# Kernel tuning notes

Measured on AMD Instinct MI355X. Metric: run time of the kernel, lower is better.

Reference implementation:

```python
import jax, jax.numpy as jnp
import numpy as np

B, L, E, H, NUM_USERS = 4096, 64, 384, 256, 10000
EPS = 1e-5


def _ln(x, g, b):
    m = jnp.mean(x, axis=-1, keepdims=True)
    v = jnp.mean((x - m) ** 2, axis=-1, keepdims=True)
    return g * (x - m) / jnp.sqrt(v + EPS) + b


def setup_inputs() -> dict:
    key = jax.random.key(0)
    ks = iter(jax.random.split(key, 32))
    inp = {}
    inp['user_ids'] = jax.random.randint(next(ks), (B,), 0, NUM_USERS)
    inp['query_embeddings'] = jax.random.normal(next(ks), (B, E), dtype=jnp.float32)
    inp['llm_embeddings'] = jax.random.normal(next(ks), (L, E), dtype=jnp.float32)
    inp['emb_table'] = jax.random.normal(next(ks), (NUM_USERS, E), dtype=jnp.float32) * 0.02
    # GNN layer 0 projections (E->H) for user/query/llm node types
    s0 = 1.0 / np.sqrt(E)
    for t in ('u', 'q', 'l'):
        inp[f'W{t}0'] = jax.random.uniform(next(ks), (E, H), jnp.float32, -s0, s0)
        inp[f'b{t}0'] = jnp.zeros((H,), jnp.float32)
    inp['g0'] = jnp.ones((H,), jnp.float32)
    inp['be0'] = jnp.zeros((H,), jnp.float32)
    # GNN layer 1 projections (H->H)
    s1 = 1.0 / np.sqrt(H)
    for t in ('u', 'q', 'l'):
        inp[f'W{t}1'] = jax.random.uniform(next(ks), (H, H), jnp.float32, -s1, s1)
        inp[f'b{t}1'] = jnp.zeros((H,), jnp.float32)
    inp['g1'] = jnp.ones((H,), jnp.float32)
    inp['be1'] = jnp.zeros((H,), jnp.float32)
    # prediction MLP: Linear(2H->H), ReLU, Linear(H->1)
    s2 = 1.0 / np.sqrt(2 * H)
    inp['w1'] = jax.random.uniform(next(ks), (2 * H, H), jnp.float32, -s2, s2)
    inp['b1'] = jnp.zeros((H,), jnp.float32)
    s3 = 1.0 / np.sqrt(H)
    inp['w2'] = jax.random.uniform(next(ks), (H, 1), jnp.float32, -s3, s3)
    inp['b2'] = jnp.zeros((1,), jnp.float32)
    return inp


def _gnn_block(x, W, b, g, be):
    # adjacency only targets 'turn' (absent), so the layer collapses to:
    # x_proj = Linear(x); out = LayerNorm(dropout(x_proj) + x_proj)  (eval: dropout=id)
    xp = x @ W + b
    return _ln(xp + xp, g, be)


def reference(user_ids, query_embeddings, llm_embeddings, emb_table,
              Wu0, bu0, Wq0, bq0, Wl0, bl0, g0, be0,
              Wu1, bu1, Wq1, bq1, Wl1, bl1, g1, be1,
              w1, b1, w2, b2):
    u = emb_table[user_ids]                      # [B, E]
    q = query_embeddings                         # [B, E]
    l = llm_embeddings                           # [L, E]
    # GNN layer 0
    u = _gnn_block(u, Wu0, bu0, g0, be0)
    q = _gnn_block(q, Wq0, bq0, g0, be0)
    l = _gnn_block(l, Wl0, bl0, g0, be0)
    # GNN layer 1
    u = _gnn_block(u, Wu1, bu1, g1, be1)
    q = _gnn_block(q, Wq1, bq1, g1, be1)
    l = _gnn_block(l, Wl1, bl1, g1, be1)
    uq = u + q                                   # [B, H]
    nb, nl = uq.shape[0], l.shape[0]
    combined = jnp.concatenate([
        jnp.broadcast_to(l[None, :, :], (nb, nl, l.shape[-1])),
        jnp.broadcast_to(uq[:, None, :], (nb, nl, uq.shape[-1])),
    ], axis=-1)                                  # [B, L, 2H]
    h = jax.nn.relu(combined @ w1 + b1)          # [B, L, H]
    scores = (h @ w2 + b2)[..., 0]               # [B, L]
    return scores
```

## Files before the change

kernel.cpp:

```cpp
#include <hip/hip_runtime.h>

constexpr float EPS_LN = 1e-5f;

using f32x4 = __attribute__((ext_vector_type(4))) float;
using s16x8 = __attribute__((ext_vector_type(8))) short;

__device__ __forceinline__ short f2bf(float f) {
  union { float f; unsigned u; } v; v.f = f;
  unsigned r = v.u + 0x7fff + ((v.u >> 16) & 1);
  return (short)(r >> 16);
}

__device__ __forceinline__ s16x8 cvt8(float4 a, float4 b) {
  s16x8 r;
  r[0] = f2bf(a.x); r[1] = f2bf(a.y); r[2] = f2bf(a.z); r[3] = f2bf(a.w);
  r[4] = f2bf(b.x); r[5] = f2bf(b.y); r[6] = f2bf(b.z); r[7] = f2bf(b.w);
  return r;
}

#define MFMA(a, b, c) __builtin_amdgcn_mfma_f32_16x16x32_bf16((a), (b), (c), 0, 0, 0)

__device__ __forceinline__ void gld_lds16(const void* g, void* l) {
  __builtin_amdgcn_global_load_lds(
      (const __attribute__((address_space(1))) unsigned int*)g,
      (__attribute__((address_space(3))) unsigned int*)l, 16, 0, 0);
}

struct P {
  const int* uid;
  const float *qe, *le, *tab;
  const float *Wu0, *bu0, *Wq0, *bq0, *Wl0, *bl0, *g0, *be0;
  const float *Wu1, *bu1, *Wq1, *bq1, *Wl1, *bl1, *g1, *be1;
  const float *w1, *b1, *w2, *b2;
  short *wt0u, *wt0q, *wt0l, *wt1u, *wt1q, *wt1l, *w1tU, *w1tL;
  short *y0, *uqB;
  float *lw, *out;
};

template<int NK>
__device__ __forceinline__ void dgemm(const short* __restrict__ wt,
                                      const s16x8* aF, int lg, int lr, int c0,
                                      f32x4 acc[4]) {
  #pragma unroll
  for (int kk = 0; kk < NK; ++kk) {
    const short* base = wt + (size_t)kk * 8192 + (size_t)(lg * 256 + c0 + lr) * 8;
    #pragma unroll
    for (int n = 0; n < 4; ++n) {
      const s16x8 bf = *(const s16x8*)(base + n * 128);
      acc[n] = MFMA(aF[kk], bf, acc[n]);
    }
  }
}

__device__ __forceinline__ void ln16(float z[4][4], int tid, int w, int lr, int lg,
                                     int c0, const float* __restrict__ g,
                                     const float* __restrict__ be,
                                     float (*ssum)[16], float (*ssq)[16],
                                     float* mub, float* rsb) {
  __syncthreads();
  float s1[4] = {0, 0, 0, 0}, s2[4] = {0, 0, 0, 0};
  #pragma unroll
  for (int n = 0; n < 4; ++n)
    #pragma unroll
    for (int r = 0; r < 4; ++r) { s1[r] += z[n][r]; s2[r] += z[n][r] * z[n][r]; }
  #pragma unroll
  for (int off = 1; off < 16; off <<= 1)
    #pragma unroll
    for (int r = 0; r < 4; ++r) {
      s1[r] += __shfl_xor(s1[r], off, 64);
      s2[r] += __shfl_xor(s2[r], off, 64);
    }
  if (lr == 0) {
    #pragma unroll
    for (int r = 0; r < 4; ++r) { ssum[w][lg * 4 + r] = s1[r]; ssq[w][lg * 4 + r] = s2[r]; }
  }
  __syncthreads();
  if (tid < 16) {
    float S1 = 0, S2 = 0;
    #pragma unroll
    for (int ww = 0; ww < 4; ++ww) { S1 += ssum[ww][tid]; S2 += ssq[ww][tid]; }
    float mu = S1 * (1.f / 256.f);
    float var = S2 * (1.f / 256.f) - mu * mu;
    mub[tid] = mu;
    rsb[tid] = rsqrtf(var + EPS_LN);
  }
  __syncthreads();
  #pragma unroll
  for (int n = 0; n < 4; ++n) {
    const int c = c0 + n * 16 + lr;
    const float gv = g[c], bv = be[c];
    #pragma unroll
    for (int r = 0; r < 4; ++r) {
      const int rr = lg * 4 + r;
      z[n][r] = gv * (z[n][r] - mub[rr]) * rsb[rr] + bv;
    }
  }
}

__device__ __forceinline__ void bias2(const f32x4 acc[4], const float* __restrict__ b,
                                      int c0, int lr, float z[4][4]) {
  #pragma unroll
  for (int n = 0; n < 4; ++n) {
    const float bv = b[c0 + n * 16 + lr];
    #pragma unroll
    for (int r = 0; r < 4; ++r) z[n][r] = 2.f * (acc[n][r] + bv);
  }
}

__device__ __forceinline__ void store_y(const float z[4][4], short* y_s,
                                        int c0, int lr, int lg) {
  #pragma unroll
  for (int n = 0; n < 4; ++n)
    #pragma unroll
    for (int r = 0; r < 4; ++r)
      y_s[(lg * 4 + r) * 264 + c0 + n * 16 + lr] = f2bf(z[n][r]);
}

__device__ __forceinline__ void load_aF(const short* y_s, s16x8* aF, int lr, int lg) {
  #pragma unroll
  for (int kk = 0; kk < 8; ++kk)
    aF[kk] = *(const s16x8*)&y_s[lr * 264 + kk * 32 + lg * 8];
}

__global__ __launch_bounds__(256) void k0_kernel(P p) {
  __shared__ float tile[64][65];
  int bx = blockIdx.x;
  const int tid = threadIdx.x;
  const float* src;
  short* dst;
  int rowoff = 0;
  if (bx < 72) {
    const int m = bx / 24; bx -= m * 24;
    src = (m == 0) ? p.Wu0 : (m == 1) ? p.Wq0 : p.Wl0;
    dst = (m == 0) ? p.wt0u : (m == 1) ? p.wt0q : p.wt0l;
  } else if (bx < 120) {
    bx -= 72; const int m = bx / 16; bx -= m * 16;
    src = (m == 0) ? p.Wu1 : (m == 1) ? p.Wq1 : p.Wl1;
    dst = (m == 0) ? p.wt1u : (m == 1) ? p.wt1q : p.wt1l;
  } else if (bx < 136) {
    bx -= 120; src = p.w1; dst = p.w1tL;
  } else {
    bx -= 136; src = p.w1; dst = p.w1tU; rowoff = 256;
  }
  const int tn = bx & 3, tk = bx >> 2;
  {
    const int r = tid >> 2, cq = (tid & 3) * 16;
    const float* s = src + (size_t)(rowoff + tk * 64 + r) * 256 + tn * 64 + cq;
    #pragma unroll
    for (int j = 0; j < 4; ++j) {
      float4 v = *(const float4*)(s + j * 4);
      tile[r][cq + j * 4 + 0] = v.x; tile[r][cq + j * 4 + 1] = v.y;
      tile[r][cq + j * 4 + 2] = v.z; tile[r][cq + j * 4 + 3] = v.w;
    }
  }
  __syncthreads();
  {
    const int nn = tid >> 2, kq = (tid & 3) * 16;
    const int n = tn * 64 + nn;
    #pragma unroll
    for (int h = 0; h < 2; ++h) {
      const int kl = kq + h * 8;
      const int kglob = tk * 64 + kl;
      const int kk = kglob >> 5, kg = (kglob & 31) >> 3;
      s16x8 v;
      #pragma unroll
      for (int ko = 0; ko < 8; ++ko) v[ko] = f2bf(tile[kl + ko][nn]);
      *(s16x8*)(dst + ((size_t)(kk * 4 + kg) * 256 + n) * 8) = v;
    }
  }
}

__global__ __launch_bounds__(256) void ka_kernel(P p) {
  __shared__ __align__(16) short y_s[16 * 264];
  __shared__ float ssum[4][16], ssq[4][16], mub[16], rsb[16];
  const int tid = threadIdx.x, w = tid >> 6, lane = tid & 63;
  const int lr = lane & 15, lg = lane >> 4;
  const int c0 = w * 64;
  const int t = blockIdx.x;
  const int r0 = t * 16;
  const float* arow;
  const short* wt;
  const float* bias;
  if (t < 256)      { arow = p.tab + (size_t)p.uid[r0 + lr] * 384; wt = p.wt0u; bias = p.bu0; }
  else if (t < 512) { arow = p.qe + (size_t)(r0 - 4096 + lr) * 384; wt = p.wt0q; bias = p.bq0; }
  else              { arow = p.le + (size_t)((t - 512) * 16 + lr) * 384; wt = p.wt0l; bias = p.bl0; }
  s16x8 aF[12];
  #pragma unroll
  for (int kk = 0; kk < 12; ++kk)
    aF[kk] = cvt8(*(const float4*)(arow + kk * 32 + lg * 8),
                  *(const float4*)(arow + kk * 32 + lg * 8 + 4));
  const f32x4 z4 = {0.f, 0.f, 0.f, 0.f};
  f32x4 acc[4] = {z4, z4, z4, z4};
  dgemm<12>(wt, aF, lg, lr, c0, acc);
  float z[4][4];
  bias2(acc, bias, c0, lr, z);
  ln16(z, tid, w, lr, lg, c0, p.g0, p.be0, ssum, ssq, mub, rsb);
  store_y(z, y_s, c0, lr, lg);
  __syncthreads();
  #pragma unroll
  for (int i = 0; i < 2; ++i) {
    const int idx = i * 256 + tid;
    const int row = idx >> 5, cc = (idx & 31) * 8;
    *(s16x8*)(p.y0 + (size_t)(r0 + row) * 256 + cc) = *(const s16x8*)&y_s[row * 264 + cc];
  }
}

__global__ __launch_bounds__(256) void kb_kernel(P p) {
  __shared__ __align__(16) short y_s[16 * 264];
  __shared__ float ssum[4][16], ssq[4][16], mub[16], rsb[16];
  const int tid = threadIdx.x, w = tid >> 6, lane = tid & 63;
  const int lr = lane & 15, lg = lane >> 4;
  const int c0 = w * 64;
  const int bx = blockIdx.x;
  const f32x4 z4 = {0.f, 0.f, 0.f, 0.f};

  if (bx < 256) {
    const int r0 = bx * 16;
    s16x8 aF[8];
    {
      const s16x8* ap = (const s16x8*)(p.y0 + (size_t)(r0 + lr) * 256);
      #pragma unroll
      for (int kk = 0; kk < 8; ++kk) aF[kk] = ap[kk * 4 + lg];
    }
    f32x4 accU[4] = {z4, z4, z4, z4};
    dgemm<8>(p.wt1u, aF, lg, lr, c0, accU);
    {
      const s16x8* ap = (const s16x8*)(p.y0 + (size_t)(4096 + r0 + lr) * 256);
      #pragma unroll
      for (int kk = 0; kk < 8; ++kk) aF[kk] = ap[kk * 4 + lg];
    }
    f32x4 accQ[4] = {z4, z4, z4, z4};
    dgemm<8>(p.wt1q, aF, lg, lr, c0, accQ);
    float z[4][4], zq[4][4];
    bias2(accU, p.bu1, c0, lr, z);
    ln16(z, tid, w, lr, lg, c0, p.g1, p.be1, ssum, ssq, mub, rsb);
    bias2(accQ, p.bq1, c0, lr, zq);
    ln16(zq, tid, w, lr, lg, c0, p.g1, p.be1, ssum, ssq, mub, rsb);
    #pragma unroll
    for (int n = 0; n < 4; ++n)
      #pragma unroll
      for (int r = 0; r < 4; ++r) z[n][r] += zq[n][r];
    store_y(z, y_s, c0, lr, lg);
    __syncthreads();
    #pragma unroll
    for (int i = 0; i < 2; ++i) {
      const int idx = i * 256 + tid;
      const int row = idx >> 5, cc = (idx & 31) * 8;
      *(s16x8*)(p.uqB + (size_t)(r0 + row) * 256 + cc) = *(const s16x8*)&y_s[row * 264 + cc];
    }
  } else {
    const int rb = (bx - 256) * 16;
    s16x8 aF[8];
    {
      const s16x8* ap = (const s16x8*)(p.y0 + (size_t)(8192 + rb + lr) * 256);
      #pragma unroll
      for (int kk = 0; kk < 8; ++kk) aF[kk] = ap[kk * 4 + lg];
    }
    f32x4 acc[4] = {z4, z4, z4, z4};
    dgemm<8>(p.wt1l, aF, lg, lr, c0, acc);
    float z[4][4];
    bias2(acc, p.bl1, c0, lr, z);
    ln16(z, tid, w, lr, lg, c0, p.g1, p.be1, ssum, ssq, mub, rsb);
    store_y(z, y_s, c0, lr, lg);
    __syncthreads();
    load_aF(y_s, aF, lr, lg);
    #pragma unroll
    for (int n = 0; n < 4; ++n) acc[n] = z4;
    dgemm<8>(p.w1tL, aF, lg, lr, c0, acc);
    #pragma unroll
    for (int n = 0; n < 4; ++n) {
      const int c = c0 + n * 16 + lr;
      const float bv = p.b1[c];
      #pragma unroll
      for (int r = 0; r < 4; ++r)
        p.lw[(size_t)(rb + lg * 4 + r) * 256 + c] = acc[n][r] + bv;
    }
  }
}

__global__ __launch_bounds__(256, 1) void kc_kernel(P p) {
  __shared__ __align__(16) float lw_s[64 * 256];
  __shared__ __align__(16) float uqw_s[16 * 260];
  __shared__ float w2s[256];
  const int tid = threadIdx.x, w = tid >> 6, lane = tid & 63;
  const int lr = lane & 15, lg = lane >> 4;
  const int c0 = w * 64;
  const int r0 = blockIdx.x * 16;

  #pragma unroll
  for (int s = 0; s < 16; ++s) {
    const int i = w * 16 + s;
    gld_lds16(p.lw + (size_t)i * 256 + ((lane ^ (i & 7)) << 2),
              (char*)lw_s + (size_t)i * 1024);
  }
  __builtin_amdgcn_sched_barrier(0);
  w2s[tid] = p.w2[tid];

  s16x8 aF[8];
  {
    const s16x8* ap = (const s16x8*)(p.uqB + (size_t)(r0 + lr) * 256);
    #pragma unroll
    for (int kk = 0; kk < 8; ++kk) aF[kk] = ap[kk * 4 + lg];
  }
  const f32x4 z4 = {0.f, 0.f, 0.f, 0.f};
  f32x4 acc[4] = {z4, z4, z4, z4};
  dgemm<8>(p.w1tU, aF, lg, lr, c0, acc);
  #pragma unroll
  for (int n = 0; n < 4; ++n)
    #pragma unroll
    for (int r = 0; r < 4; ++r)
      uqw_s[(lg * 4 + r) * 260 + c0 + n * 16 + lr] = acc[n][r];
  __syncthreads();

  const float b2v = p.b2[0];
  const int l = lane;
  float sacc[4] = {0.f, 0.f, 0.f, 0.f};
  #pragma unroll 4
  for (int jj = 0; jj < 64; ++jj) {
    const float4 lwv = *(const float4*)&lw_s[l * 256 + ((jj ^ (l & 7)) << 2)];
    const float4 w2v = *(const float4*)&w2s[jj * 4];
    #pragma unroll
    for (int bi = 0; bi < 4; ++bi) {
      const float4 uqv = *(const float4*)&uqw_s[(w * 4 + bi) * 260 + jj * 4];
      sacc[bi] += fmaxf(lwv.x + uqv.x, 0.f) * w2v.x;
      sacc[bi] += fmaxf(lwv.y + uqv.y, 0.f) * w2v.y;
      sacc[bi] += fmaxf(lwv.z + uqv.z, 0.f) * w2v.z;
      sacc[bi] += fmaxf(lwv.w + uqv.w, 0.f) * w2v.w;
    }
  }
  #pragma unroll
  for (int bi = 0; bi < 4; ++bi)
    p.out[(size_t)(r0 + w * 4 + bi) * 64 + l] = sacc[bi] + b2v;
}

extern "C" void kernel_launch(void* const* d_in, const int* in_sizes, int n_in,
                              void* d_out, int out_size, void* d_ws, size_t ws_size,
                              hipStream_t stream) {
  (void)in_sizes; (void)n_in; (void)out_size; (void)ws_size;
  P p;
  p.uid = (const int*)d_in[0];
  p.qe  = (const float*)d_in[1];
  p.le  = (const float*)d_in[2];
  p.tab = (const float*)d_in[3];
  p.Wu0 = (const float*)d_in[4];  p.bu0 = (const float*)d_in[5];
  p.Wq0 = (const float*)d_in[6];  p.bq0 = (const float*)d_in[7];
  p.Wl0 = (const float*)d_in[8];  p.bl0 = (const float*)d_in[9];
  p.g0  = (const float*)d_in[10]; p.be0 = (const float*)d_in[11];
  p.Wu1 = (const float*)d_in[12]; p.bu1 = (const float*)d_in[13];
  p.Wq1 = (const float*)d_in[14]; p.bq1 = (const float*)d_in[15];
  p.Wl1 = (const float*)d_in[16]; p.bl1 = (const float*)d_in[17];
  p.g1  = (const float*)d_in[18]; p.be1 = (const float*)d_in[19];
  p.w1  = (const float*)d_in[20]; p.b1  = (const float*)d_in[21];
  p.w2  = (const float*)d_in[22]; p.b2  = (const float*)d_in[23];

  short* wsS = (short*)d_ws;
  size_t o = 0;
  p.wt0u = wsS + o; o += 98304;
  p.wt0q = wsS + o; o += 98304;
  p.wt0l = wsS + o; o += 98304;
  p.wt1u = wsS + o; o += 65536;
  p.wt1q = wsS + o; o += 65536;
  p.wt1l = wsS + o; o += 65536;
  p.w1tU = wsS + o; o += 65536;
  p.w1tL = wsS + o; o += 65536;
  p.y0   = wsS + o; o += 2113536;
  p.uqB  = wsS + o; o += 1048576;
  p.lw   = (float*)(wsS + o);
  p.out  = (float*)d_out;

  hipLaunchKernelGGL(k0_kernel, dim3(152), dim3(256), 0, stream, p);
  hipLaunchKernelGGL(ka_kernel, dim3(516), dim3(256), 0, stream, p);
  hipLaunchKernelGGL(kb_kernel, dim3(260), dim3(256), 0, stream, p);
  hipLaunchKernelGGL(kc_kernel, dim3(256), dim3(256), 0, stream, p);
}
```

Baseline: 50.34 us.

## Fuse four kernel launches into one persistent cooperative kernel with grid syncs

Turns the four phase kernels (weight transpose/convert, layer 0, layer 1, MLP score) into device functions and runs them from a single cooperative kernel of 256 blocks, with grid.sync between phases and a shared-memory union. This removes three kernel-launch boundaries and their drain/ramp gaps. In exchange, each grid-wide barrier has its own cost, the ka phase now runs 516 tiles on 256 blocks (about three rounds, with the third round mostly idle), and occupancy is capped at one block per CU by the largest shared-memory footprint. If the cooperative launch fails, it falls back to the original four launches.

```diff
diff --git a/kernel.cpp b/kernel.cpp
--- a/kernel.cpp
+++ b/kernel.cpp
@@ -1,4 +1,5 @@
 #include <hip/hip_runtime.h>
+#include <hip/hip_cooperative_groups.h>
 
 constexpr float EPS_LN = 1e-5f;
 
@@ -37,6 +38,18 @@
   float *lw, *out;
 };
 
+struct __align__(16) SM_P0 { float tile[64][65]; };
+struct __align__(16) SM_PA {
+  short y_s[16 * 264];
+  float ssum[4][16], ssq[4][16], mub[16], rsb[16];
+};
+struct __align__(16) SM_PC {
+  float lw_s[64 * 256];
+  float uqw_s[16 * 260];
+  float w2s[256];
+};
+union __align__(16) SMU { SM_P0 p0; SM_PA pa; SM_PC pc; };
+
 template<int NK>
 __device__ __forceinline__ void dgemm(const short* __restrict__ wt,
                                       const s16x8* aF, int lg, int lr, int c0,
@@ -122,10 +135,7 @@
     aF[kk] = *(const s16x8*)&y_s[lr * 264 + kk * 32 + lg * 8];
 }
 
-__global__ __launch_bounds__(256) void k0_kernel(P p) {
-  __shared__ float tile[64][65];
-  int bx = blockIdx.x;
-  const int tid = threadIdx.x;
+__device__ __forceinline__ void phase_k0(const P& p, int bx, int tid, SM_P0& s) {
   const float* src;
   short* dst;
   int rowoff = 0;
@@ -145,12 +155,12 @@
   const int tn = bx & 3, tk = bx >> 2;
   {
     const int r = tid >> 2, cq = (tid & 3) * 16;
-    const float* s = src + (size_t)(rowoff + tk * 64 + r) * 256 + tn * 64 + cq;
+    const float* sp = src + (size_t)(rowoff + tk * 64 + r) * 256 + tn * 64 + cq;
     #pragma unroll
     for (int j = 0; j < 4; ++j) {
-      float4 v = *(const float4*)(s + j * 4);
-      tile[r][cq + j * 4 + 0] = v.x; tile[r][cq + j * 4 + 1] = v.y;
-      tile[r][cq + j * 4 + 2] = v.z; tile[r][cq + j * 4 + 3] = v.w;
+      float4 v = *(const float4*)(sp + j * 4);
+      s.tile[r][cq + j * 4 + 0] = v.x; s.tile[r][cq + j * 4 + 1] = v.y;
+      s.tile[r][cq + j * 4 + 2] = v.z; s.tile[r][cq + j * 4 + 3] = v.w;
     }
   }
   __syncthreads();
@@ -164,19 +174,16 @@
       const int kk = kglob >> 5, kg = (kglob & 31) >> 3;
       s16x8 v;
       #pragma unroll
-      for (int ko = 0; ko < 8; ++ko) v[ko] = f2bf(tile[kl + ko][nn]);
+      for (int ko = 0; ko < 8; ++ko) v[ko] = f2bf(s.tile[kl + ko][nn]);
       *(s16x8*)(dst + ((size_t)(kk * 4 + kg) * 256 + n) * 8) = v;
     }
   }
 }
 
-__global__ __launch_bounds__(256) void ka_kernel(P p) {
-  __shared__ __align__(16) short y_s[16 * 264];
-  __shared__ float ssum[4][16], ssq[4][16], mub[16], rsb[16];
-  const int tid = threadIdx.x, w = tid >> 6, lane = tid & 63;
+__device__ __forceinline__ void phase_ka(const P& p, int t, int tid, SM_PA& s) {
+  const int w = tid >> 6, lane = tid & 63;
   const int lr = lane & 15, lg = lane >> 4;
   const int c0 = w * 64;
-  const int t = blockIdx.x;
   const int r0 = t * 16;
   const float* arow;
   const short* wt;
@@ -194,24 +201,21 @@
   dgemm<12>(wt, aF, lg, lr, c0, acc);
   float z[4][4];
   bias2(acc, bias, c0, lr, z);
-  ln16(z, tid, w, lr, lg, c0, p.g0, p.be0, ssum, ssq, mub, rsb);
-  store_y(z, y_s, c0, lr, lg);
+  ln16(z, tid, w, lr, lg, c0, p.g0, p.be0, s.ssum, s.ssq, s.mub, s.rsb);
+  store_y(z, s.y_s, c0, lr, lg);
   __syncthreads();
   #pragma unroll
   for (int i = 0; i < 2; ++i) {
     const int idx = i * 256 + tid;
     const int row = idx >> 5, cc = (idx & 31) * 8;
-    *(s16x8*)(p.y0 + (size_t)(r0 + row) * 256 + cc) = *(const s16x8*)&y_s[row * 264 + cc];
-  }
-}
-
-__global__ __launch_bounds__(256) void kb_kernel(P p) {
-  __shared__ __align__(16) short y_s[16 * 264];
-  __shared__ float ssum[4][16], ssq[4][16], mub[16], rsb[16];
-  const int tid = threadIdx.x, w = tid >> 6, lane = tid & 63;
+    *(s16x8*)(p.y0 + (size_t)(r0 + row) * 256 + cc) = *(const s16x8*)&s.y_s[row * 264 + cc];
+  }
+}
+
+__device__ __forceinline__ void phase_kb(const P& p, int bx, int tid, SM_PA& s) {
+  const int w = tid >> 6, lane = tid & 63;
   const int lr = lane & 15, lg = lane >> 4;
   const int c0 = w * 64;
-  const int bx = blockIdx.x;
   const f32x4 z4 = {0.f, 0.f, 0.f, 0.f};
 
   if (bx < 256) {
@@ -233,20 +237,20 @@
     dgemm<8>(p.wt1q, aF, lg, lr, c0, accQ);
     float z[4][4], zq[4][4];
     bias2(accU, p.bu1, c0, lr, z);
-    ln16(z, tid, w, lr, lg, c0, p.g1, p.be1, ssum, ssq, mub, rsb);
+    ln16(z, tid, w, lr, lg, c0, p.g1, p.be1, s.ssum, s.ssq, s.mub, s.rsb);
     bias2(accQ, p.bq1, c0, lr, zq);
-    ln16(zq, tid, w, lr, lg, c0, p.g1, p.be1, ssum, ssq, mub, rsb);
+    ln16(zq, tid, w, lr, lg, c0, p.g1, p.be1, s.ssum, s.ssq, s.mub, s.rsb);
     #pragma unroll
     for (int n = 0; n < 4; ++n)
       #pragma unroll
       for (int r = 0; r < 4; ++r) z[n][r] += zq[n][r];
-    store_y(z, y_s, c0, lr, lg);
+    store_y(z, s.y_s, c0, lr, lg);
     __syncthreads();
     #pragma unroll
     for (int i = 0; i < 2; ++i) {
       const int idx = i * 256 + tid;
       const int row = idx >> 5, cc = (idx & 31) * 8;
-      *(s16x8*)(p.uqB + (size_t)(r0 + row) * 256 + cc) = *(const s16x8*)&y_s[row * 264 + cc];
+      *(s16x8*)(p.uqB + (size_t)(r0 + row) * 256 + cc) = *(const s16x8*)&s.y_s[row * 264 + cc];
     }
   } else {
     const int rb = (bx - 256) * 16;
@@ -260,10 +264,10 @@
     dgemm<8>(p.wt1l, aF, lg, lr, c0, acc);
     float z[4][4];
     bias2(acc, p.bl1, c0, lr, z);
-    ln16(z, tid, w, lr, lg, c0, p.g1, p.be1, ssum, ssq, mub, rsb);
-    store_y(z, y_s, c0, lr, lg);
+    ln16(z, tid, w, lr, lg, c0, p.g1, p.be1, s.ssum, s.ssq, s.mub, s.rsb);
+    store_y(z, s.y_s, c0, lr, lg);
     __syncthreads();
-    load_aF(y_s, aF, lr, lg);
+    load_aF(s.y_s, aF, lr, lg);
     #pragma unroll
     for (int n = 0; n < 4; ++n) acc[n] = z4;
     dgemm<8>(p.w1tL, aF, lg, lr, c0, acc);
@@ -278,23 +282,20 @@
   }
 }
 
-__global__ __launch_bounds__(256, 1) void kc_kernel(P p) {
-  __shared__ __align__(16) float lw_s[64 * 256];
-  __shared__ __align__(16) float uqw_s[16 * 260];
-  __shared__ float w2s[256];
-  const int tid = threadIdx.x, w = tid >> 6, lane = tid & 63;
+__device__ __forceinline__ void phase_kc(const P& p, int bx, int tid, SM_PC& s) {
+  const int w = tid >> 6, lane = tid & 63;
   const int lr = lane & 15, lg = lane >> 4;
   const int c0 = w * 64;
-  const int r0 = blockIdx.x * 16;
-
-  #pragma unroll
-  for (int s = 0; s < 16; ++s) {
-    const int i = w * 16 + s;
+  const int r0 = bx * 16;
+
+  #pragma unroll
+  for (int st = 0; st < 16; ++st) {
+    const int i = w * 16 + st;
     gld_lds16(p.lw + (size_t)i * 256 + ((lane ^ (i & 7)) << 2),
-              (char*)lw_s + (size_t)i * 1024);
+              (char*)s.lw_s + (size_t)i * 1024);
   }
   __builtin_amdgcn_sched_barrier(0);
-  w2s[tid] = p.w2[tid];
+  s.w2s[tid] = p.w2[tid];
 
   s16x8 aF[8];
   {
@@ -309,7 +310,7 @@
   for (int n = 0; n < 4; ++n)
     #pragma unroll
     for (int r = 0; r < 4; ++r)
-      uqw_s[(lg * 4 + r) * 260 + c0 + n * 16 + lr] = acc[n][r];
+      s.uqw_s[(lg * 4 + r) * 260 + c0 + n * 16 + lr] = acc[n][r];
   __syncthreads();
 
   const float b2v = p.b2[0];
@@ -317,11 +318,11 @@
   float sacc[4] = {0.f, 0.f, 0.f, 0.f};
   #pragma unroll 4
   for (int jj = 0; jj < 64; ++jj) {
-    const float4 lwv = *(const float4*)&lw_s[l * 256 + ((jj ^ (l & 7)) << 2)];
-    const float4 w2v = *(const float4*)&w2s[jj * 4];
+    const float4 lwv = *(const float4*)&s.lw_s[l * 256 + ((jj ^ (l & 7)) << 2)];
+    const float4 w2v = *(const float4*)&s.w2s[jj * 4];
     #pragma unroll
     for (int bi = 0; bi < 4; ++bi) {
-      const float4 uqv = *(const float4*)&uqw_s[(w * 4 + bi) * 260 + jj * 4];
+      const float4 uqv = *(const float4*)&s.uqw_s[(w * 4 + bi) * 260 + jj * 4];
       sacc[bi] += fmaxf(lwv.x + uqv.x, 0.f) * w2v.x;
       sacc[bi] += fmaxf(lwv.y + uqv.y, 0.f) * w2v.y;
       sacc[bi] += fmaxf(lwv.z + uqv.z, 0.f) * w2v.z;
@@ -331,6 +332,47 @@
   #pragma unroll
   for (int bi = 0; bi < 4; ++bi)
     p.out[(size_t)(r0 + w * 4 + bi) * 64 + l] = sacc[bi] + b2v;
+}
+
+__global__ __launch_bounds__(256, 1) void fused_kernel(P p) {
+  __shared__ SMU sm;
+  const int tid = threadIdx.x;
+  const int bid = blockIdx.x;
+  cooperative_groups::grid_group grid = cooperative_groups::this_grid();
+
+  for (int j = bid; j < 152; j += 256) {
+    phase_k0(p, j, tid, sm.p0);
+    __syncthreads();
+  }
+  grid.sync();
+  for (int j = bid; j < 516; j += 256) {
+    phase_ka(p, j, tid, sm.pa);
+    __syncthreads();
+  }
+  grid.sync();
+  for (int j = bid; j < 260; j += 256) {
+    phase_kb(p, j, tid, sm.pa);
+    __syncthreads();
+  }
+  grid.sync();
+  phase_kc(p, bid, tid, sm.pc);
+}
+
+__global__ __launch_bounds__(256) void k0_kernel(P p) {
+  __shared__ SM_P0 s;
+  phase_k0(p, blockIdx.x, threadIdx.x, s);
+}
+__global__ __launch_bounds__(256) void ka_kernel(P p) {
+  __shared__ SM_PA s;
+  phase_ka(p, blockIdx.x, threadIdx.x, s);
+}
+__global__ __launch_bounds__(256) void kb_kernel(P p) {
+  __shared__ SM_PA s;
+  phase_kb(p, blockIdx.x, threadIdx.x, s);
+}
+__global__ __launch_bounds__(256, 1) void kc_kernel(P p) {
+  __shared__ SM_PC s;
+  phase_kc(p, blockIdx.x, threadIdx.x, s);
 }
 
 extern "C" void kernel_launch(void* const* d_in, const int* in_sizes, int n_in,
@@ -368,8 +410,13 @@
   p.lw   = (float*)(wsS + o);
   p.out  = (float*)d_out;
 
-  hipLaunchKernelGGL(k0_kernel, dim3(152), dim3(256), 0, stream, p);
-  hipLaunchKernelGGL(ka_kernel, dim3(516), dim3(256), 0, stream, p);
-  hipLaunchKernelGGL(kb_kernel, dim3(260), dim3(256), 0, stream, p);
-  hipLaunchKernelGGL(kc_kernel, dim3(256), dim3(256), 0, stream, p);
-}
+  void* kargs[] = { (void*)&p };
+  hipError_t err = hipLaunchCooperativeKernel((void*)fused_kernel, dim3(256),
+                                              dim3(256), kargs, 0, stream);
+  if (err != hipSuccess) {
+    hipLaunchKernelGGL(k0_kernel, dim3(152), dim3(256), 0, stream, p);
+    hipLaunchKernelGGL(ka_kernel, dim3(516), dim3(256), 0, stream, p);
+    hipLaunchKernelGGL(kb_kernel, dim3(260), dim3(256), 0, stream, p);
+    hipLaunchKernelGGL(kc_kernel, dim3(256), dim3(256), 0, stream, p);
+  }
+}
```

Result: slower. 163.1 us (+224.0%).

## Fuse GNN layers 0 and 1 into one kernel, sum user/query in consumer

Applied to the files above, without the earlier changes.

Merges the layer-0 and layer-1 kernels so each 16-row block runs both GEMM+LayerNorm stages back to back, passing the intermediate through LDS instead of a global y0 buffer. User and query rows are now handled by separate blocks, each writing its own bf16 output, and the u+q sum moves into the prediction kernel's operand load. This removes one launch and the global round trip of the intermediate activations. In exchange kc reads two buffers, and the bf16 sum adds an extra rounding step.

```diff
diff --git a/kernel.cpp b/kernel.cpp
--- a/kernel.cpp
+++ b/kernel.cpp
@@ -9,6 +9,11 @@
   union { float f; unsigned u; } v; v.f = f;
   unsigned r = v.u + 0x7fff + ((v.u >> 16) & 1);
   return (short)(r >> 16);
+}
+__device__ __forceinline__ float bf2f(short h) {
+  union { unsigned u; float f; } v;
+  v.u = ((unsigned)(unsigned short)h) << 16;
+  return v.f;
 }
 
 __device__ __forceinline__ s16x8 cvt8(float4 a, float4 b) {
@@ -33,7 +38,7 @@
   const float *Wu1, *bu1, *Wq1, *bq1, *Wl1, *bl1, *g1, *be1;
   const float *w1, *b1, *w2, *b2;
   short *wt0u, *wt0q, *wt0l, *wt1u, *wt1q, *wt1l, *w1tU, *w1tL;
-  short *y0, *uqB;
+  short *uqU, *uqQ;
   float *lw, *out;
 };
 
@@ -170,42 +175,7 @@
   }
 }
 
-__global__ __launch_bounds__(256) void ka_kernel(P p) {
-  __shared__ __align__(16) short y_s[16 * 264];
-  __shared__ float ssum[4][16], ssq[4][16], mub[16], rsb[16];
-  const int tid = threadIdx.x, w = tid >> 6, lane = tid & 63;
-  const int lr = lane & 15, lg = lane >> 4;
-  const int c0 = w * 64;
-  const int t = blockIdx.x;
-  const int r0 = t * 16;
-  const float* arow;
-  const short* wt;
-  const float* bias;
-  if (t < 256)      { arow = p.tab + (size_t)p.uid[r0 + lr] * 384; wt = p.wt0u; bias = p.bu0; }
-  else if (t < 512) { arow = p.qe + (size_t)(r0 - 4096 + lr) * 384; wt = p.wt0q; bias = p.bq0; }
-  else              { arow = p.le + (size_t)((t - 512) * 16 + lr) * 384; wt = p.wt0l; bias = p.bl0; }
-  s16x8 aF[12];
-  #pragma unroll
-  for (int kk = 0; kk < 12; ++kk)
-    aF[kk] = cvt8(*(const float4*)(arow + kk * 32 + lg * 8),
-                  *(const float4*)(arow + kk * 32 + lg * 8 + 4));
-  const f32x4 z4 = {0.f, 0.f, 0.f, 0.f};
-  f32x4 acc[4] = {z4, z4, z4, z4};
-  dgemm<12>(wt, aF, lg, lr, c0, acc);
-  float z[4][4];
-  bias2(acc, bias, c0, lr, z);
-  ln16(z, tid, w, lr, lg, c0, p.g0, p.be0, ssum, ssq, mub, rsb);
-  store_y(z, y_s, c0, lr, lg);
-  __syncthreads();
-  #pragma unroll
-  for (int i = 0; i < 2; ++i) {
-    const int idx = i * 256 + tid;
-    const int row = idx >> 5, cc = (idx & 31) * 8;
-    *(s16x8*)(p.y0 + (size_t)(r0 + row) * 256 + cc) = *(const s16x8*)&y_s[row * 264 + cc];
-  }
-}
-
-__global__ __launch_bounds__(256) void kb_kernel(P p) {
+__global__ __launch_bounds__(256) void kab_kernel(P p) {
   __shared__ __align__(16) short y_s[16 * 264];
   __shared__ float ssum[4][16], ssq[4][16], mub[16], rsb[16];
   const int tid = threadIdx.x, w = tid >> 6, lane = tid & 63;
@@ -214,59 +184,73 @@
   const int bx = blockIdx.x;
   const f32x4 z4 = {0.f, 0.f, 0.f, 0.f};
 
-  if (bx < 256) {
-    const int r0 = bx * 16;
-    s16x8 aF[8];
-    {
-      const s16x8* ap = (const s16x8*)(p.y0 + (size_t)(r0 + lr) * 256);
-      #pragma unroll
-      for (int kk = 0; kk < 8; ++kk) aF[kk] = ap[kk * 4 + lg];
-    }
-    f32x4 accU[4] = {z4, z4, z4, z4};
-    dgemm<8>(p.wt1u, aF, lg, lr, c0, accU);
-    {
-      const s16x8* ap = (const s16x8*)(p.y0 + (size_t)(4096 + r0 + lr) * 256);
-      #pragma unroll
-      for (int kk = 0; kk < 8; ++kk) aF[kk] = ap[kk * 4 + lg];
-    }
-    f32x4 accQ[4] = {z4, z4, z4, z4};
-    dgemm<8>(p.wt1q, aF, lg, lr, c0, accQ);
-    float z[4][4], zq[4][4];
-    bias2(accU, p.bu1, c0, lr, z);
+  if (bx < 512) {
+    const bool isq = bx >= 256;
+    const int t = bx & 255;
+    const int r0 = t * 16;
+    const float* arow = isq ? p.qe + (size_t)(r0 + lr) * 384
+                            : p.tab + (size_t)p.uid[r0 + lr] * 384;
+    const short* wt0 = isq ? p.wt0q : p.wt0u;
+    const float* b0  = isq ? p.bq0 : p.bu0;
+    const short* wt1 = isq ? p.wt1q : p.wt1u;
+    const float* b1v = isq ? p.bq1 : p.bu1;
+    short* outB      = isq ? p.uqQ : p.uqU;
+
+    s16x8 aF[12];
+    #pragma unroll
+    for (int kk = 0; kk < 12; ++kk)
+      aF[kk] = cvt8(*(const float4*)(arow + kk * 32 + lg * 8),
+                    *(const float4*)(arow + kk * 32 + lg * 8 + 4));
+    f32x4 acc[4] = {z4, z4, z4, z4};
+    dgemm<12>(wt0, aF, lg, lr, c0, acc);
+    float z[4][4];
+    bias2(acc, b0, c0, lr, z);
+    ln16(z, tid, w, lr, lg, c0, p.g0, p.be0, ssum, ssq, mub, rsb);
+    store_y(z, y_s, c0, lr, lg);
+    __syncthreads();
+    s16x8 aH[8];
+    load_aF(y_s, aH, lr, lg);
+    #pragma unroll
+    for (int n = 0; n < 4; ++n) acc[n] = z4;
+    dgemm<8>(wt1, aH, lg, lr, c0, acc);
+    bias2(acc, b1v, c0, lr, z);
     ln16(z, tid, w, lr, lg, c0, p.g1, p.be1, ssum, ssq, mub, rsb);
-    bias2(accQ, p.bq1, c0, lr, zq);
-    ln16(zq, tid, w, lr, lg, c0, p.g1, p.be1, ssum, ssq, mub, rsb);
-    #pragma unroll
-    for (int n = 0; n < 4; ++n)
-      #pragma unroll
-      for (int r = 0; r < 4; ++r) z[n][r] += zq[n][r];
     store_y(z, y_s, c0, lr, lg);
     __syncthreads();
     #pragma unroll
     for (int i = 0; i < 2; ++i) {
       const int idx = i * 256 + tid;
       const int row = idx >> 5, cc = (idx & 31) * 8;
-      *(s16x8*)(p.uqB + (size_t)(r0 + row) * 256 + cc) = *(const s16x8*)&y_s[row * 264 + cc];
+      *(s16x8*)(outB + (size_t)(r0 + row) * 256 + cc) = *(const s16x8*)&y_s[row * 264 + cc];
     }
   } else {
-    const int rb = (bx - 256) * 16;
-    s16x8 aF[8];
-    {
-      const s16x8* ap = (const s16x8*)(p.y0 + (size_t)(8192 + rb + lr) * 256);
-      #pragma unroll
-      for (int kk = 0; kk < 8; ++kk) aF[kk] = ap[kk * 4 + lg];
-    }
+    const int rb = (bx - 512) * 16;
+    const float* arow = p.le + (size_t)(rb + lr) * 384;
+    s16x8 aF[12];
+    #pragma unroll
+    for (int kk = 0; kk < 12; ++kk)
+      aF[kk] = cvt8(*(const float4*)(arow + kk * 32 + lg * 8),
+                    *(const float4*)(arow + kk * 32 + lg * 8 + 4));
     f32x4 acc[4] = {z4, z4, z4, z4};
-    dgemm<8>(p.wt1l, aF, lg, lr, c0, acc);
+    dgemm<12>(p.wt0l, aF, lg, lr, c0, acc);
     float z[4][4];
+    bias2(acc, p.bl0, c0, lr, z);
+    ln16(z, tid, w, lr, lg, c0, p.g0, p.be0, ssum, ssq, mub, rsb);
+    store_y(z, y_s, c0, lr, lg);
+    __syncthreads();
+    s16x8 aH[8];
+    load_aF(y_s, aH, lr, lg);
+    #pragma unroll
+    for (int n = 0; n < 4; ++n) acc[n] = z4;
+    dgemm<8>(p.wt1l, aH, lg, lr, c0, acc);
     bias2(acc, p.bl1, c0, lr, z);
     ln16(z, tid, w, lr, lg, c0, p.g1, p.be1, ssum, ssq, mub, rsb);
     store_y(z, y_s, c0, lr, lg);
     __syncthreads();
-    load_aF(y_s, aF, lr, lg);
+    load_aF(y_s, aH, lr, lg);
     #pragma unroll
     for (int n = 0; n < 4; ++n) acc[n] = z4;
-    dgemm<8>(p.w1tL, aF, lg, lr, c0, acc);
+    dgemm<8>(p.w1tL, aH, lg, lr, c0, acc);
     #pragma unroll
     for (int n = 0; n < 4; ++n) {
       const int c = c0 + n * 16 + lr;
@@ -298,9 +282,16 @@
 
   s16x8 aF[8];
   {
-    const s16x8* ap = (const s16x8*)(p.uqB + (size_t)(r0 + lr) * 256);
-    #pragma unroll
-    for (int kk = 0; kk < 8; ++kk) aF[kk] = ap[kk * 4 + lg];
+    const s16x8* pu = (const s16x8*)(p.uqU + (size_t)(r0 + lr) * 256);
+    const s16x8* pq = (const s16x8*)(p.uqQ + (size_t)(r0 + lr) * 256);
+    #pragma unroll
+    for (int kk = 0; kk < 8; ++kk) {
+      const s16x8 a = pu[kk * 4 + lg], b = pq[kk * 4 + lg];
+      s16x8 o;
+      #pragma unroll
+      for (int j = 0; j < 8; ++j) o[j] = f2bf(bf2f(a[j]) + bf2f(b[j]));
+      aF[kk] = o;
+    }
   }
   const f32x4 z4 = {0.f, 0.f, 0.f, 0.f};
   f32x4 acc[4] = {z4, z4, z4, z4};
@@ -363,13 +354,12 @@
   p.wt1l = wsS + o; o += 65536;
   p.w1tU = wsS + o; o += 65536;
   p.w1tL = wsS + o; o += 65536;
-  p.y0   = wsS + o; o += 2113536;
-  p.uqB  = wsS + o; o += 1048576;
+  p.uqU  = wsS + o; o += 1048576;
+  p.uqQ  = wsS + o; o += 1048576;
   p.lw   = (float*)(wsS + o);
   p.out  = (float*)d_out;
 
   hipLaunchKernelGGL(k0_kernel, dim3(152), dim3(256), 0, stream, p);
-  hipLaunchKernelGGL(ka_kernel, dim3(516), dim3(256), 0, stream, p);
-  hipLaunchKernelGGL(kb_kernel, dim3(260), dim3(256), 0, stream, p);
+  hipLaunchKernelGGL(kab_kernel, dim3(516), dim3(256), 0, stream, p);
   hipLaunchKernelGGL(kc_kernel, dim3(256), dim3(256), 0, stream, p);
 }
```

Result: faster. 49.08 us (-2.5%).
